# Kernel tuning notes

Hardware: AMD Instinct MI355X
Metric: run time of the kernel (lower is better)

Reference implementation:

```python
import jax, jax.numpy as jnp
import numpy as np

N_NODES = 131072
N_EDGES = 262144
N_GRAPHS = 4096
EMB = 300
N_LAYERS = 5
N_TASKS = 12
N_EXPERTS = 8
GATE_DIM = 300
NUM_ATOM_TYPE = 120
NUM_CHIRALITY = 3
NUM_BOND_TYPE = 6
NUM_BOND_DIR = 3


def setup_inputs() -> dict:
    key = jax.random.key(0)
    ks = jax.random.split(key, 24)
    x = jnp.stack([
        jax.random.randint(ks[0], (N_NODES,), 0, NUM_ATOM_TYPE),
        jax.random.randint(ks[1], (N_NODES,), 0, NUM_CHIRALITY),
    ], axis=1)
    edge_index = jax.random.randint(ks[2], (2, N_EDGES), 0, N_NODES)
    edge_attr = jnp.stack([
        jax.random.randint(ks[3], (N_EDGES,), 0, NUM_BOND_TYPE),
        jax.random.randint(ks[4], (N_EDGES,), 0, NUM_BOND_DIR),
    ], axis=1)
    batch = jnp.sort(jax.random.randint(ks[5], (N_NODES,), 0, N_GRAPHS))

    s = 0.05
    atom_emb1 = jax.random.normal(ks[6], (NUM_ATOM_TYPE, EMB)) * s
    atom_emb2 = jax.random.normal(ks[7], (NUM_CHIRALITY, EMB)) * s
    edge_emb1 = jax.random.normal(ks[8], (N_LAYERS, NUM_BOND_TYPE, EMB)) * s
    edge_emb2 = jax.random.normal(ks[9], (N_LAYERS, NUM_BOND_DIR, EMB)) * s
    mlp_w1 = jax.random.normal(ks[10], (N_LAYERS, EMB, 2 * EMB)) * s
    mlp_b1 = jnp.zeros((N_LAYERS, 2 * EMB))
    mlp_w2 = jax.random.normal(ks[11], (N_LAYERS, 2 * EMB, EMB)) * s
    mlp_b2 = jnp.zeros((N_LAYERS, EMB))
    bn_gamma = jnp.ones((N_LAYERS, EMB))
    bn_beta = jnp.zeros((N_LAYERS, EMB))
    gate_w1 = jax.random.normal(ks[12], (EMB, GATE_DIM)) * s
    gate_b1 = jnp.zeros((GATE_DIM,))
    gate_bn_g = jnp.ones((GATE_DIM,))
    gate_bn_b = jnp.zeros((GATE_DIM,))
    gate_w2 = jax.random.normal(ks[13], (GATE_DIM, GATE_DIM)) * s
    gate_b2 = jnp.zeros((GATE_DIM,))
    cluster = jax.random.normal(ks[14], (N_EXPERTS, GATE_DIM)) * s
    experts_w = jax.random.normal(ks[15], (EMB, N_TASKS * N_EXPERTS)) * s
    experts_b = jnp.zeros((N_TASKS * N_EXPERTS,))
    return dict(x=x, edge_index=edge_index, edge_attr=edge_attr, batch=batch,
                atom_emb1=atom_emb1, atom_emb2=atom_emb2,
                edge_emb1=edge_emb1, edge_emb2=edge_emb2,
                mlp_w1=mlp_w1, mlp_b1=mlp_b1, mlp_w2=mlp_w2, mlp_b2=mlp_b2,
                bn_gamma=bn_gamma, bn_beta=bn_beta,
                gate_w1=gate_w1, gate_b1=gate_b1,
                gate_bn_g=gate_bn_g, gate_bn_b=gate_bn_b,
                gate_w2=gate_w2, gate_b2=gate_b2,
                cluster=cluster, experts_w=experts_w, experts_b=experts_b)


def _batchnorm(h, g, b, eps=1e-5):
    mu = h.mean(axis=0)
    var = h.var(axis=0)
    return g * (h - mu) * jax.lax.rsqrt(var + eps) + b


def _forward(x, edge_index, edge_attr, batch,
             atom_emb1, atom_emb2, edge_emb1, edge_emb2,
             mlp_w1, mlp_b1, mlp_w2, mlp_b2, bn_gamma, bn_beta,
             gate_w1, gate_b1, gate_bn_g, gate_bn_b, gate_w2, gate_b2,
             cluster, experts_w, experts_b):
    n = x.shape[0]
    src, dst = edge_index[0], edge_index[1]
    ea0, ea1 = edge_attr[:, 0], edge_attr[:, 1]
    # node input embedding
    h = atom_emb1[x[:, 0]] + atom_emb2[x[:, 1]]  # [N, EMB]
    n_layers = mlp_w1.shape[0]
    for l in range(n_layers):
        ee = edge_emb1[l][ea0] + edge_emb2[l][ea1]  # [E, EMB]
        # self loops: attr = (bond_type=4, dir=0) for every node
        self_ee = edge_emb1[l][4] + edge_emb2[l][0]  # [EMB]
        agg = jax.ops.segment_sum(h[src] + ee, dst, num_segments=n)
        agg = agg + h + self_ee  # self-loop messages
        hid = jax.nn.relu(agg @ mlp_w1[l] + mlp_b1[l])
        h = hid @ mlp_w2[l] + mlp_b2[l]
        h = _batchnorm(h, bn_gamma[l], bn_beta[l])
        if l < n_layers - 1:
            h = jax.nn.relu(h)
    # graph pooling (JK='last')
    sums = jax.ops.segment_sum(h, batch, num_segments=N_GRAPHS)  # [B, EMB]
    counts = jax.ops.segment_sum(jnp.ones((n, 1), h.dtype), batch, num_segments=N_GRAPHS)
    gnn_out = sums / jnp.maximum(counts, 1.0)  # mean pool
    gate_input = sums  # global_add_pool
    # experts head: sum(gnn_out[:, :, None] * W, dim=1) + b == gnn_out @ W + b
    n_experts = cluster.shape[0]
    clf_logit = (gnn_out @ experts_w + experts_b).reshape(N_GRAPHS, -1, n_experts)
    # gate network
    zh = _batchnorm(gate_input @ gate_w1 + gate_b1, gate_bn_g, gate_bn_b)
    z = jax.nn.relu(zh) @ gate_w2 + gate_b2  # [B, GATE_DIM]
    # q: temperature-scaled softmax over cosine similarity to cluster centroids
    zn = z / jnp.maximum(jnp.linalg.norm(z, axis=1, keepdims=True), 1e-6)
    cn = cluster / jnp.maximum(jnp.linalg.norm(cluster, axis=1, keepdims=True), 1e-6)
    q = jax.nn.softmax(10.0 * (zn @ cn.T), axis=-1)  # T = 10
    return clf_logit, z, q


def reference(x, edge_index, edge_attr, batch,
              atom_emb1, atom_emb2, edge_emb1, edge_emb2,
              mlp_w1, mlp_b1, mlp_w2, mlp_b2, bn_gamma, bn_beta,
              gate_w1, gate_b1, gate_bn_g, gate_bn_b, gate_w2, gate_b2,
              cluster, experts_w, experts_b):
    return _forward(x, edge_index, edge_attr, batch,
                    atom_emb1, atom_emb2, edge_emb1, edge_emb2,
                    mlp_w1, mlp_b1, mlp_w2, mlp_b2, bn_gamma, bn_beta,
                    gate_w1, gate_b1, gate_bn_g, gate_bn_b, gate_w2, gate_b2,
                    cluster, experts_w, experts_b)
```

## Files before the change

kernel.cpp:

```cpp
#include <hip/hip_runtime.h>
#include <hip/hip_bf16.h>

typedef unsigned short u16;
typedef unsigned int u32;

#define NN 131072
#define NE 262144
#define NG 4096
#define EMB 300
#define HID 600
#define NL 5
#define NTNE 96
#define NEXP 8

#define W1T_ROWS 640
#define W1T_K    328
#define W2T_ROWS 384
#define W2T_K    648
#define EE_S     304

typedef __attribute__((ext_vector_type(8)))  short  s16x8;
typedef __attribute__((ext_vector_type(8)))  __bf16 b16x8;
typedef __attribute__((ext_vector_type(16))) float  f32x16;

static __device__ __forceinline__ float u2f(u16 u) {
    union { u32 i; float f; } w; w.i = ((u32)u) << 16; return w.f;
}
static __device__ __forceinline__ u16 f2u(float f) {
    union { float f; u32 i; } w; w.f = f;
    return (u16)((w.i + 0x7fffu + ((w.i >> 16) & 1u)) >> 16);
}

static __device__ __forceinline__ f32x16 mfma_3216(s16x8 a, s16x8 b, f32x16 c) {
    return __builtin_amdgcn_mfma_f32_32x32x16_bf16(
        __builtin_bit_cast(b16x8, a), __builtin_bit_cast(b16x8, b), c, 0, 0, 0);
}

__global__ void k_zero(float* __restrict__ p, int n) {
    int i = blockIdx.x * 256 + threadIdx.x;
    if (i < n) p[i] = 0.f;
}
__global__ void k_zero_int(int* __restrict__ p, int n) {
    int i = blockIdx.x * 256 + threadIdx.x;
    if (i < n) p[i] = 0;
}

__global__ void k_embed(const int* __restrict__ x, const float* __restrict__ ae1,
                        const float* __restrict__ ae2, u16* __restrict__ h) {
    int i = blockIdx.x;
    int a0 = x[2 * i], a1 = x[2 * i + 1];
    for (int f = threadIdx.x; f < EMB; f += blockDim.x)
        h[(size_t)i * EMB + f] = f2u(ae1[a0 * EMB + f] + ae2[a1 * EMB + f]);
}

__global__ void k_hist(const int* __restrict__ ei, int* __restrict__ deg) {
    int e = blockIdx.x * 256 + threadIdx.x;
    if (e < NE) atomicAdd(&deg[ei[NE + e]], 1);
}

__global__ __launch_bounds__(1024) void k_scan(const int* __restrict__ deg,
                                               int* __restrict__ rowstart) {
    __shared__ int lds[1024];
    int tid = threadIdx.x;
    int base = tid * 128;
    int s = 0;
    for (int j = 0; j < 128; ++j) s += deg[base + j];
    lds[tid] = s;
    __syncthreads();
    for (int off = 1; off < 1024; off <<= 1) {
        int v = (tid >= off) ? lds[tid - off] : 0;
        __syncthreads();
        lds[tid] += v;
        __syncthreads();
    }
    int run = (tid == 0) ? 0 : lds[tid - 1];
    for (int j = 0; j < 128; ++j) {
        rowstart[base + j] = run;
        run += deg[base + j];
    }
    if (tid == 1023) rowstart[NN] = run;
}

__global__ void k_fill(const int* __restrict__ ei, const int* __restrict__ ea,
                       int* __restrict__ deg, const int* __restrict__ rowstart,
                       u32* __restrict__ payload) {
    int e = blockIdx.x * 256 + threadIdx.x;
    if (e >= NE) return;
    int src = ei[e], dst = ei[NE + e];
    int c = ea[2 * e] * 3 + ea[2 * e + 1];
    int old = atomicSub(&deg[dst], 1);
    int pos = rowstart[dst] + old - 1;
    payload[pos] = (u32)src | ((u32)c << 17);
}

__global__ void k_prep_w1(const float* __restrict__ w1, u16* __restrict__ w1t) {
    int n = blockIdx.x;
    int l = blockIdx.y;
    size_t dst = ((size_t)l * W1T_ROWS + n) * W1T_K;
    for (int k = threadIdx.x; k < W1T_K; k += blockDim.x) {
        u16 v = 0;
        if (n < HID && k < EMB) v = f2u(w1[(size_t)l * EMB * HID + (size_t)k * HID + n]);
        w1t[dst + k] = v;
    }
}
__global__ void k_prep_w2(const float* __restrict__ w2, u16* __restrict__ w2t) {
    int n = blockIdx.x;
    int l = blockIdx.y;
    size_t dst = ((size_t)l * W2T_ROWS + n) * W2T_K;
    for (int k = threadIdx.x; k < W2T_K; k += blockDim.x) {
        u16 v = 0;
        if (n < EMB && k < HID) v = f2u(w2[(size_t)l * HID * EMB + (size_t)k * EMB + n]);
        w2t[dst + k] = v;
    }
}

__global__ void k_prep_ee(const float* __restrict__ ee1, const float* __restrict__ ee2,
                          u16* __restrict__ eeT) {
    int c = blockIdx.x;
    int l = blockIdx.y;
    size_t dst = ((size_t)l * 18 + c) * EE_S;
    const float* e1 = ee1 + (size_t)l * 6 * EMB + (c / 3) * EMB;
    const float* e2 = ee2 + (size_t)l * 3 * EMB + (c % 3) * EMB;
    for (int f = threadIdx.x; f < EE_S; f += blockDim.x)
        eeT[dst + f] = (f < EMB) ? f2u(e1[f] + e2[f]) : (u16)0;
}

__global__ void k_prep_bn(const float* __restrict__ stats, const float* __restrict__ bg,
                          const float* __restrict__ bb, float invM,
                          u16* __restrict__ scT, u16* __restrict__ shT) {
    int t = threadIdx.x;
    if (t >= EE_S) return;
    if (t < EMB) {
        float mu = stats[t] * invM;
        float var = stats[EMB + t] * invM - mu * mu;
        float sc = bg[t] * rsqrtf(var + 1e-5f);
        scT[t] = f2u(sc);
        shT[t] = f2u(bb[t] - mu * sc);
    } else {
        scT[t] = 0; shT[t] = 0;
    }
}

template <bool APPLY_BN>
__global__ __launch_bounds__(512) void k_layer1(const u16* __restrict__ h,
                                                const u32* __restrict__ payload,
                                                const int* __restrict__ rowstart,
                                                const u16* __restrict__ eeT,
                                                const u16* __restrict__ scT,
                                                const u16* __restrict__ shT,
                                                const u16* __restrict__ w1t,
                                                const float* __restrict__ b1,
                                                u16* __restrict__ hid) {
    __shared__ __align__(16) u16 A_s[64 * 328];
    int tid = threadIdx.x;
    int lane = tid & 63, wid = tid >> 6;
    int wr = wid >> 2, wc = wid & 3;
    int l31 = lane & 31, lhi = lane >> 5;
    size_t rowBase = (size_t)blockIdx.x * 64;

    for (int idx = tid; idx < 64 * 28; idx += 512)
        A_s[(idx / 28) * 328 + 300 + (idx % 28)] = 0;
    __syncthreads();

    for (int task = tid; task < 32 * 75; task += 512) {
        int pr = task / 75, fc = task - pr * 75;
        int f0 = fc * 4;
        int iA = (int)rowBase + pr;
        int iB = iA + 32;
        int begA = rowstart[iA], endA = rowstart[iA + 1];
        int begB = rowstart[iB], endB = rowstart[iB + 1];
        float sc0 = 1.f, sc1 = 1.f, sc2 = 1.f, sc3 = 1.f;
        float sh0 = 0.f, sh1 = 0.f, sh2 = 0.f, sh3 = 0.f;
        if (APPLY_BN) {
            ushort4 scv = *(const ushort4*)&scT[f0];
            ushort4 shv = *(const ushort4*)&shT[f0];
            sc0 = u2f(scv.x); sc1 = u2f(scv.y); sc2 = u2f(scv.z); sc3 = u2f(scv.w);
            sh0 = u2f(shv.x); sh1 = u2f(shv.y); sh2 = u2f(shv.z); sh3 = u2f(shv.w);
        }
        ushort4 ev = *(const ushort4*)&eeT[12 * EE_S + f0];
        float e0 = u2f(ev.x), e1v = u2f(ev.y), e2v = u2f(ev.z), e3 = u2f(ev.w);

        ushort4 hvA = *(const ushort4*)&h[(size_t)iA * EMB + f0];
        ushort4 hvB = *(const ushort4*)&h[(size_t)iB * EMB + f0];
        float vA0 = u2f(hvA.x), vA1 = u2f(hvA.y), vA2 = u2f(hvA.z), vA3 = u2f(hvA.w);
        float vB0 = u2f(hvB.x), vB1 = u2f(hvB.y), vB2 = u2f(hvB.z), vB3 = u2f(hvB.w);
        if (APPLY_BN) {
            vA0 = fmaxf(vA0 * sc0 + sh0, 0.f); vB0 = fmaxf(vB0 * sc0 + sh0, 0.f);
            vA1 = fmaxf(vA1 * sc1 + sh1, 0.f); vB1 = fmaxf(vB1 * sc1 + sh1, 0.f);
            vA2 = fmaxf(vA2 * sc2 + sh2, 0.f); vB2 = fmaxf(vB2 * sc2 + sh2, 0.f);
            vA3 = fmaxf(vA3 * sc3 + sh3, 0.f); vB3 = fmaxf(vB3 * sc3 + sh3, 0.f);
        }
        vA0 += e0; vA1 += e1v; vA2 += e2v; vA3 += e3;
        vB0 += e0; vB1 += e1v; vB2 += e2v; vB3 += e3;

        int eA = begA, eB = begB;
        while (eA < endA && eB < endB) {
            u32 pA = payload[eA], pB = payload[eB];
            int sA = pA & 0x1FFFF, sB = pB & 0x1FFFF;
            ushort4 svA = *(const ushort4*)&h[(size_t)sA * EMB + f0];
            ushort4 svB = *(const ushort4*)&h[(size_t)sB * EMB + f0];
            ushort4 ecA = *(const ushort4*)&eeT[(size_t)(pA >> 17) * EE_S + f0];
            ushort4 ecB = *(const ushort4*)&eeT[(size_t)(pB >> 17) * EE_S + f0];
            float gA0 = u2f(svA.x), gA1 = u2f(svA.y), gA2 = u2f(svA.z), gA3 = u2f(svA.w);
            float gB0 = u2f(svB.x), gB1 = u2f(svB.y), gB2 = u2f(svB.z), gB3 = u2f(svB.w);
            if (APPLY_BN) {
                gA0 = fmaxf(gA0 * sc0 + sh0, 0.f); gB0 = fmaxf(gB0 * sc0 + sh0, 0.f);
                gA1 = fmaxf(gA1 * sc1 + sh1, 0.f); gB1 = fmaxf(gB1 * sc1 + sh1, 0.f);
                gA2 = fmaxf(gA2 * sc2 + sh2, 0.f); gB2 = fmaxf(gB2 * sc2 + sh2, 0.f);
                gA3 = fmaxf(gA3 * sc3 + sh3, 0.f); gB3 = fmaxf(gB3 * sc3 + sh3, 0.f);
            }
            vA0 += gA0 + u2f(ecA.x); vB0 += gB0 + u2f(ecB.x);
            vA1 += gA1 + u2f(ecA.y); vB1 += gB1 + u2f(ecB.y);
            vA2 += gA2 + u2f(ecA.z); vB2 += gB2 + u2f(ecB.z);
            vA3 += gA3 + u2f(ecA.w); vB3 += gB3 + u2f(ecB.w);
            ++eA; ++eB;
        }
        for (; eA < endA; ++eA) {
            u32 p = payload[eA];
            int src = p & 0x1FFFF;
            ushort4 sv = *(const ushort4*)&h[(size_t)src * EMB + f0];
            ushort4 ec = *(const ushort4*)&eeT[(size_t)(p >> 17) * EE_S + f0];
            float g0 = u2f(sv.x), g1 = u2f(sv.y), g2 = u2f(sv.z), g3 = u2f(sv.w);
            if (APPLY_BN) {
                g0 = fmaxf(g0 * sc0 + sh0, 0.f);
                g1 = fmaxf(g1 * sc1 + sh1, 0.f);
                g2 = fmaxf(g2 * sc2 + sh2, 0.f);
                g3 = fmaxf(g3 * sc3 + sh3, 0.f);
            }
            vA0 += g0 + u2f(ec.x);
            vA1 += g1 + u2f(ec.y);
            vA2 += g2 + u2f(ec.z);
            vA3 += g3 + u2f(ec.w);
        }
        for (; eB < endB; ++eB) {
            u32 p = payload[eB];
            int src = p & 0x1FFFF;
            ushort4 sv = *(const ushort4*)&h[(size_t)src * EMB + f0];
            ushort4 ec = *(const ushort4*)&eeT[(size_t)(p >> 17) * EE_S + f0];
            float g0 = u2f(sv.x), g1 = u2f(sv.y), g2 = u2f(sv.z), g3 = u2f(sv.w);
            if (APPLY_BN) {
                g0 = fmaxf(g0 * sc0 + sh0, 0.f);
                g1 = fmaxf(g1 * sc1 + sh1, 0.f);
                g2 = fmaxf(g2 * sc2 + sh2, 0.f);
                g3 = fmaxf(g3 * sc3 + sh3, 0.f);
            }
            vB0 += g0 + u2f(ec.x);
            vB1 += g1 + u2f(ec.y);
            vB2 += g2 + u2f(ec.z);
            vB3 += g3 + u2f(ec.w);
        }
        short4 oA, oB;
        oA.x = (short)f2u(vA0); oA.y = (short)f2u(vA1);
        oA.z = (short)f2u(vA2); oA.w = (short)f2u(vA3);
        oB.x = (short)f2u(vB0); oB.y = (short)f2u(vB1);
        oB.z = (short)f2u(vB2); oB.w = (short)f2u(vB3);
        *(short4*)&A_s[pr * 328 + f0] = oA;
        *(short4*)&A_s[(pr + 32) * 328 + f0] = oB;
    }
    __syncthreads();

    s16x8 afr[20];
    int abase = (wr * 32 + l31) * 328 + lhi * 8;
#pragma unroll
    for (int s = 0; s < 20; ++s) afr[s] = *(const s16x8*)&A_s[abase + s * 16];

    for (int c5 = 0; c5 < 5; ++c5) {
        int col = c5 * 128 + wc * 32 + l31;
        const u16* bp = w1t + (size_t)col * W1T_K + lhi * 8;
        f32x16 acc = {};
#pragma unroll
        for (int s = 0; s < 20; ++s)
            acc = mfma_3216(afr[s], *(const s16x8*)&bp[s * 16], acc);
        if (col < HID) {
            float bias = b1[col];
#pragma unroll
            for (int r = 0; r < 16; ++r) {
                int row = (r & 3) + 8 * (r >> 2) + 4 * lhi;
                hid[(rowBase + wr * 32 + row) * HID + col] =
                    f2u(fmaxf(acc[r] + bias, 0.f));
            }
        }
    }
}

__global__ __launch_bounds__(256) void k_gemm2(const u16* __restrict__ hid,
                                               const u16* __restrict__ w2t,
                                               const float* __restrict__ b2,
                                               u16* __restrict__ hout) {
    __shared__ __align__(16) u16 A_s[64 * 72];
    __shared__ __align__(16) u16 B_s[128 * 72];
    int tid = threadIdx.x;
    int lane = tid & 63, wid = tid >> 6;
    int wr = wid >> 1, wc = wid & 1;
    int l31 = lane & 31, lhi = lane >> 5;
    size_t rowBase = (size_t)blockIdx.x * 64;
    int cc = blockIdx.y * 128;

    f32x16 acc0 = {}, acc1 = {};
    int aoff = (wr * 32 + l31) * 72 + lhi * 8;
    int boff0 = (wc * 64 + l31) * 72 + lhi * 8;
    int boff1 = boff0 + 32 * 72;

    for (int sl = 0; sl < 10; ++sl) {
        int k0 = sl * 64;
        for (int idx = tid; idx < 512; idx += 256) {
            int m = idx >> 3, kv = idx & 7;
            int k = k0 + kv * 8;
            s16x8 v = {};
            if (k < HID) v = *(const s16x8*)&hid[(rowBase + m) * HID + k];
            *(s16x8*)&A_s[m * 72 + kv * 8] = v;
        }
        for (int idx = tid; idx < 1024; idx += 256) {
            int n = idx >> 3, kv = idx & 7;
            *(s16x8*)&B_s[n * 72 + kv * 8] =
                *(const s16x8*)&w2t[(size_t)(cc + n) * W2T_K + k0 + kv * 8];
        }
        __syncthreads();

        int smax = (sl < 9) ? 4 : 2;
        for (int s = 0; s < smax; ++s) {
            s16x8 a  = *(const s16x8*)&A_s[aoff + s * 16];
            s16x8 ba = *(const s16x8*)&B_s[boff0 + s * 16];
            s16x8 bb = *(const s16x8*)&B_s[boff1 + s * 16];
            acc0 = mfma_3216(a, ba, acc0);
            acc1 = mfma_3216(a, bb, acc1);
        }
        __syncthreads();
    }

    int colA = cc + wc * 64 + l31;
    int colB = colA + 32;
    if (colA < EMB) {
        float bias = b2[colA];
#pragma unroll
        for (int r = 0; r < 16; ++r) {
            int row = (r & 3) + 8 * (r >> 2) + 4 * lhi;
            hout[(rowBase + wr * 32 + row) * EMB + colA] = f2u(acc0[r] + bias);
        }
    }
    if (colB < EMB) {
        float bias = b2[colB];
#pragma unroll
        for (int r = 0; r < 16; ++r) {
            int row = (r & 3) + 8 * (r >> 2) + 4 * lhi;
            hout[(rowBase + wr * 32 + row) * EMB + colB] = f2u(acc1[r] + bias);
        }
    }
}

__global__ void k_bn_stats_h(const u16* __restrict__ X, float* __restrict__ stats) {
    int t = threadIdx.x;
    int half = t / 160;
    int pr = t - half * 160;
    if (pr >= 150) return;
    float s0 = 0.f, s1 = 0.f, q0 = 0.f, q1 = 0.f;
    for (int r = blockIdx.x * 2 + half; r < NN; r += 512) {
        u32 v = *(const u32*)&X[(size_t)r * EMB + pr * 2];
        float a = u2f((u16)(v & 0xffff));
        float b = u2f((u16)(v >> 16));
        s0 += a; s1 += b; q0 += a * a; q1 += b * b;
    }
    atomicAdd(&stats[2 * pr], s0);
    atomicAdd(&stats[2 * pr + 1], s1);
    atomicAdd(&stats[EMB + 2 * pr], q0);
    atomicAdd(&stats[EMB + 2 * pr + 1], q1);
}

template <bool RELU>
__global__ void k_bn_apply_h(u16* __restrict__ X, const float* __restrict__ stats,
                             const float* __restrict__ g, const float* __restrict__ b, float invM) {
    int r = blockIdx.x;
    for (int f = threadIdx.x; f < EMB; f += blockDim.x) {
        float mu = stats[f] * invM;
        float var = stats[EMB + f] * invM - mu * mu;
        float v = (u2f(X[(size_t)r * EMB + f]) - mu) * rsqrtf(var + 1e-5f) * g[f] + b[f];
        if (RELU) v = fmaxf(v, 0.f);
        X[(size_t)r * EMB + f] = f2u(v);
    }
}

__global__ void k_bn_stats_f(const float* __restrict__ X, int M, float* __restrict__ stats) {
    int f = threadIdx.x;
    if (f >= EMB) return;
    float s = 0.f, s2 = 0.f;
    for (int r = blockIdx.x; r < M; r += gridDim.x) {
        float v = X[(size_t)r * EMB + f];
        s += v;
        s2 += v * v;
    }
    atomicAdd(&stats[f], s);
    atomicAdd(&stats[EMB + f], s2);
}

template <bool RELU>
__global__ void k_bn_apply_f(float* __restrict__ X, const float* __restrict__ stats,
                             const float* __restrict__ g, const float* __restrict__ b, float invM) {
    int r = blockIdx.x;
    for (int f = threadIdx.x; f < EMB; f += blockDim.x) {
        float mu = stats[f] * invM;
        float var = stats[EMB + f] * invM - mu * mu;
        float v = (X[(size_t)r * EMB + f] - mu) * rsqrtf(var + 1e-5f) * g[f] + b[f];
        if (RELU) v = fmaxf(v, 0.f);
        X[(size_t)r * EMB + f] = v;
    }
}

template <bool RELU>
__global__ __launch_bounds__(256) void k_gemm(const float* __restrict__ A,
                                              const float* __restrict__ B,
                                              const float* __restrict__ bias,
                                              float* __restrict__ C, int M, int N, int K) {
    __shared__ __align__(16) float As[16][68];
    __shared__ __align__(16) float Bs[16][68];
    int tid = threadIdx.x;
    int tx = tid & 15, ty = tid >> 4;
    int rowBase = blockIdx.y * 64;
    int colBase = blockIdx.x * 64;
    float acc[4][4] = {};
    for (int k0 = 0; k0 < K; k0 += 16) {
        for (int idx = tid; idx < 1024; idx += 256) {
            int m = idx >> 4, k = idx & 15;
            int gk = k0 + k;
            As[k][m] = (gk < K) ? A[(size_t)(rowBase + m) * K + gk] : 0.f;
        }
        for (int idx = tid; idx < 1024; idx += 256) {
            int kk = idx >> 6, n = idx & 63;
            int gk = k0 + kk, gn = colBase + n;
            Bs[kk][n] = (gk < K && gn < N) ? B[(size_t)gk * N + gn] : 0.f;
        }
        __syncthreads();
#pragma unroll
        for (int k = 0; k < 16; ++k) {
            const float* ar = &As[k][ty * 4];
            const float* br = &Bs[k][tx * 4];
            float a[4], b[4];
#pragma unroll
            for (int i = 0; i < 4; ++i) a[i] = ar[i];
#pragma unroll
            for (int j = 0; j < 4; ++j) b[j] = br[j];
#pragma unroll
            for (int i = 0; i < 4; ++i)
#pragma unroll
                for (int j = 0; j < 4; ++j) acc[i][j] += a[i] * b[j];
        }
        __syncthreads();
    }
#pragma unroll
    for (int i = 0; i < 4; ++i) {
        int r = rowBase + ty * 4 + i;
#pragma unroll
        for (int j = 0; j < 4; ++j) {
            int c = colBase + tx * 4 + j;
            if (c < N && r < M) {
                float v = acc[i][j] + bias[c];
                if (RELU) v = fmaxf(v, 0.f);
                C[(size_t)r * N + c] = v;
            }
        }
    }
}

__global__ void k_pool(const u16* __restrict__ h, const int* __restrict__ batch,
                       float* __restrict__ sums, float* __restrict__ counts) {
    __shared__ int range[2];
    int g = blockIdx.x;
    int t = threadIdx.x;
    if (t < 2) {
        int target = g + t;
        int lo = 0, hi = NN;
        while (lo < hi) {
            int mid = (lo + hi) >> 1;
            if (batch[mid] < target) lo = mid + 1; else hi = mid;
        }
        range[t] = lo;
    }
    __syncthreads();
    int beg = range[0], end = range[1];
    if (t < EMB) {
        float s = 0.f;
        for (int r = beg; r < end; ++r) s += u2f(h[(size_t)r * EMB + t]);
        sums[(size_t)g * EMB + t] = s;
    }
    if (t == 0) counts[g] = (float)(end - beg);
}

__global__ void k_clf(const float* __restrict__ sums, const float* __restrict__ counts,
                      const float* __restrict__ ew, const float* __restrict__ eb,
                      float* __restrict__ out) {
    int gi = blockIdx.x;
    int t = threadIdx.x;
    if (t >= NTNE) return;
    float cnt = fmaxf(counts[gi], 1.f);
    float acc = 0.f;
    for (int k = 0; k < EMB; ++k) acc += sums[(size_t)gi * EMB + k] * ew[k * NTNE + t];
    out[(size_t)gi * NTNE + t] = acc / cnt + eb[t];
}

__global__ void k_cnorm(const float* __restrict__ cluster, float* __restrict__ cnorm) {
    int l = threadIdx.x;
    for (int e = 0; e < NEXP; ++e) {
        float s = 0.f;
        for (int f = l; f < EMB; f += 64) {
            float v = cluster[e * EMB + f];
            s += v * v;
        }
        for (int o = 32; o; o >>= 1) s += __shfl_xor(s, o);
        if (l == 0) cnorm[e] = sqrtf(s);
    }
}

__global__ void k_zout(const float* __restrict__ z, float* __restrict__ out) {
    int gi = blockIdx.x;
    for (int f = threadIdx.x; f < EMB; f += blockDim.x)
        out[(size_t)gi * EMB + f] = z[(size_t)gi * EMB + f];
}

__global__ void k_q(const float* __restrict__ z, const float* __restrict__ cluster,
                    const float* __restrict__ cnorm, float* __restrict__ qout) {
    int gi = blockIdx.x;
    int l = threadIdx.x;
    float s = 0.f;
    for (int f = l; f < EMB; f += 64) {
        float v = z[(size_t)gi * EMB + f];
        s += v * v;
    }
    for (int o = 32; o; o >>= 1) s += __shfl_xor(s, o);
    float zn = fmaxf(sqrtf(s), 1e-6f);
    float sc[NEXP];
#pragma unroll
    for (int e = 0; e < NEXP; ++e) {
        float d = 0.f;
        for (int f = l; f < EMB; f += 64) d += z[(size_t)gi * EMB + f] * cluster[e * EMB + f];
        for (int o = 32; o; o >>= 1) d += __shfl_xor(d, o);
        sc[e] = 10.f * d / (zn * fmaxf(cnorm[e], 1e-6f));
    }
    float mx = sc[0];
#pragma unroll
    for (int e = 1; e < NEXP; ++e) mx = fmaxf(mx, sc[e]);
    float se = 0.f;
#pragma unroll
    for (int e = 0; e < NEXP; ++e) {
        sc[e] = expf(sc[e] - mx);
        se += sc[e];
    }
    if (l < NEXP) qout[(size_t)gi * NEXP + l] = sc[l] / se;
}

extern "C" void kernel_launch(void* const* d_in, const int* in_sizes, int n_in,
                              void* d_out, int out_size, void* d_ws, size_t ws_size,
                              hipStream_t stream) {
    const int* x       = (const int*)d_in[0];
    const int* ei      = (const int*)d_in[1];
    const int* ea      = (const int*)d_in[2];
    const int* batch   = (const int*)d_in[3];
    const float* ae1   = (const float*)d_in[4];
    const float* ae2   = (const float*)d_in[5];
    const float* ee1   = (const float*)d_in[6];
    const float* ee2   = (const float*)d_in[7];
    const float* w1    = (const float*)d_in[8];
    const float* b1    = (const float*)d_in[9];
    const float* w2    = (const float*)d_in[10];
    const float* b2    = (const float*)d_in[11];
    const float* bng   = (const float*)d_in[12];
    const float* bnb   = (const float*)d_in[13];
    const float* gw1   = (const float*)d_in[14];
    const float* gb1   = (const float*)d_in[15];
    const float* gbng  = (const float*)d_in[16];
    const float* gbnb  = (const float*)d_in[17];
    const float* gw2   = (const float*)d_in[18];
    const float* gb2   = (const float*)d_in[19];
    const float* clus  = (const float*)d_in[20];
    const float* ew    = (const float*)d_in[21];
    const float* eb    = (const float*)d_in[22];

    char* wp = (char*)d_ws;
    u16* hbuf = (u16*)wp;                 wp += (size_t)NN * EMB * sizeof(u16);
    u16* hid = (u16*)wp;                  wp += (size_t)NN * HID * sizeof(u16);
    float* stats = (float*)wp;            wp += 2 * EMB * sizeof(float);
    u16* w1t = (u16*)wp;                  wp += (size_t)NL * W1T_ROWS * W1T_K * sizeof(u16);
    u16* w2t = (u16*)wp;                  wp += (size_t)NL * W2T_ROWS * W2T_K * sizeof(u16);
    u16* eeT = (u16*)wp;                  wp += (size_t)NL * 18 * EE_S * sizeof(u16);
    u16* scT = (u16*)wp;                  wp += EE_S * sizeof(u16);
    u16* shT = (u16*)wp;                  wp += EE_S * sizeof(u16);
    int* deg = (int*)wp;                  wp += (size_t)NN * sizeof(int);
    int* rowstart = (int*)wp;             wp += (size_t)(NN + 4) * sizeof(int);
    u32* payload = (u32*)wp;              wp += (size_t)NE * sizeof(u32);

    float* sums   = (float*)hid;
    float* counts = sums + (size_t)NG * EMB;
    float* zh     = counts + NG;
    float* zb     = zh + (size_t)NG * EMB;
    float* cnorm  = zb + (size_t)NG * EMB;

    float* out     = (float*)d_out;
    float* out_clf = out;
    float* out_z   = out + (size_t)NG * NTNE;
    float* out_q   = out_z + (size_t)NG * EMB;

    k_zero_int<<<NN / 256, 256, 0, stream>>>(deg, NN);
    k_hist<<<NE / 256, 256, 0, stream>>>(ei, deg);
    k_scan<<<1, 1024, 0, stream>>>(deg, rowstart);
    k_fill<<<NE / 256, 256, 0, stream>>>(ei, ea, deg, rowstart, payload);

    k_prep_w1<<<dim3(W1T_ROWS, NL), 64, 0, stream>>>(w1, w1t);
    k_prep_w2<<<dim3(W2T_ROWS, NL), 64, 0, stream>>>(w2, w2t);
    k_prep_ee<<<dim3(18, NL), 128, 0, stream>>>(ee1, ee2, eeT);
    k_embed<<<NN, 320, 0, stream>>>(x, ae1, ae2, hbuf);

    for (int l = 0; l < NL; ++l) {
        const u16* eeL = eeT + (size_t)l * 18 * EE_S;
        if (l == 0)
            k_layer1<false><<<NN / 64, 512, 0, stream>>>(
                hbuf, payload, rowstart, eeL, nullptr, nullptr,
                w1t + (size_t)l * W1T_ROWS * W1T_K, b1 + (size_t)l * HID, hid);
        else
            k_layer1<true><<<NN / 64, 512, 0, stream>>>(
                hbuf, payload, rowstart, eeL, scT, shT,
                w1t + (size_t)l * W1T_ROWS * W1T_K, b1 + (size_t)l * HID, hid);
        k_gemm2<<<dim3(NN / 64, 3), 256, 0, stream>>>(hid, w2t + (size_t)l * W2T_ROWS * W2T_K,
                                                      b2 + (size_t)l * EMB, hbuf);
        k_zero<<<3, 256, 0, stream>>>(stats, 2 * EMB);
        k_bn_stats_h<<<256, 320, 0, stream>>>(hbuf, stats);
        if (l < NL - 1)
            k_prep_bn<<<1, 320, 0, stream>>>(stats, bng + (size_t)l * EMB,
                                             bnb + (size_t)l * EMB, 1.f / NN, scT, shT);
    }

    k_bn_apply_h<false><<<NN, 320, 0, stream>>>(hbuf, stats, bng + (size_t)(NL - 1) * EMB,
                                                bnb + (size_t)(NL - 1) * EMB, 1.f / NN);

    k_pool<<<NG, 320, 0, stream>>>(hbuf, batch, sums, counts);
    k_clf<<<NG, 128, 0, stream>>>(sums, counts, ew, eb, out_clf);

    k_gemm<false><<<dim3(5, NG / 64), 256, 0, stream>>>(sums, gw1, gb1, zh, NG, EMB, EMB);
    k_zero<<<3, 256, 0, stream>>>(stats, 2 * EMB);
    k_bn_stats_f<<<256, 320, 0, stream>>>(zh, NG, stats);
    k_bn_apply_f<true><<<NG, 320, 0, stream>>>(zh, stats, gbng, gbnb, 1.f / NG);
    k_gemm<false><<<dim3(5, NG / 64), 256, 0, stream>>>(zh, gw2, gb2, zb, NG, EMB, EMB);

    k_cnorm<<<1, 64, 0, stream>>>(clus, cnorm);
    k_zout<<<NG, 320, 0, stream>>>(zb, out_z);
    k_q<<<NG, 64, 0, stream>>>(zb, clus, cnorm, out_q);
}
```

Before: 3.006 ms.

## Compute all output columns per gemm2 block and use nontemporal hid traffic

The second MLP GEMM now has each 64-row block compute all 384 padded output columns, with six accumulators per wave, instead of splitting columns across three blocks. Each hidden-activation tile is therefore read once rather than three times, at the cost of a 3x larger weight tile in LDS (about 64KB total), more registers, and a third as many blocks. The hidden-activation stores in gemm1 and loads in gemm2 also use nontemporal hints to reduce cache pollution.

```diff
diff --git a/kernel.cpp b/kernel.cpp
--- a/kernel.cpp
+++ b/kernel.cpp
@@ -276,8 +276,9 @@
 #pragma unroll
             for (int r = 0; r < 16; ++r) {
                 int row = (r & 3) + 8 * (r >> 2) + 4 * lhi;
-                hid[(rowBase + wr * 32 + row) * HID + col] =
-                    f2u(fmaxf(acc[r] + bias, 0.f));
+                u16 val = f2u(fmaxf(acc[r] + bias, 0.f));
+                __builtin_nontemporal_store(val,
+                    &hid[(rowBase + wr * 32 + row) * HID + col]);
             }
         }
     }
@@ -288,18 +289,16 @@
                                                const float* __restrict__ b2,
                                                u16* __restrict__ hout) {
     __shared__ __align__(16) u16 A_s[64 * 72];
-    __shared__ __align__(16) u16 B_s[128 * 72];
+    __shared__ __align__(16) u16 B_s[384 * 72];
     int tid = threadIdx.x;
     int lane = tid & 63, wid = tid >> 6;
-    int wr = wid >> 1, wc = wid & 1;
+    int wr = wid >> 1, wcg = wid & 1;
     int l31 = lane & 31, lhi = lane >> 5;
     size_t rowBase = (size_t)blockIdx.x * 64;
-    int cc = blockIdx.y * 128;
-
-    f32x16 acc0 = {}, acc1 = {};
+
+    f32x16 acc0 = {}, acc1 = {}, acc2 = {}, acc3 = {}, acc4 = {}, acc5 = {};
     int aoff = (wr * 32 + l31) * 72 + lhi * 8;
-    int boff0 = (wc * 64 + l31) * 72 + lhi * 8;
-    int boff1 = boff0 + 32 * 72;
+    int bbase = (wcg * 192 + l31) * 72 + lhi * 8;
 
     for (int sl = 0; sl < 10; ++sl) {
         int k0 = sl * 64;
@@ -307,45 +306,46 @@
             int m = idx >> 3, kv = idx & 7;
             int k = k0 + kv * 8;
             s16x8 v = {};
-            if (k < HID) v = *(const s16x8*)&hid[(rowBase + m) * HID + k];
+            if (k < HID)
+                v = __builtin_nontemporal_load(
+                        (const s16x8*)&hid[(rowBase + m) * HID + k]);
             *(s16x8*)&A_s[m * 72 + kv * 8] = v;
         }
-        for (int idx = tid; idx < 1024; idx += 256) {
+        for (int idx = tid; idx < 3072; idx += 256) {
             int n = idx >> 3, kv = idx & 7;
             *(s16x8*)&B_s[n * 72 + kv * 8] =
-                *(const s16x8*)&w2t[(size_t)(cc + n) * W2T_K + k0 + kv * 8];
+                *(const s16x8*)&w2t[(size_t)n * W2T_K + k0 + kv * 8];
         }
         __syncthreads();
 
         int smax = (sl < 9) ? 4 : 2;
         for (int s = 0; s < smax; ++s) {
-            s16x8 a  = *(const s16x8*)&A_s[aoff + s * 16];
-            s16x8 ba = *(const s16x8*)&B_s[boff0 + s * 16];
-            s16x8 bb = *(const s16x8*)&B_s[boff1 + s * 16];
-            acc0 = mfma_3216(a, ba, acc0);
-            acc1 = mfma_3216(a, bb, acc1);
+            s16x8 a = *(const s16x8*)&A_s[aoff + s * 16];
+            acc0 = mfma_3216(a, *(const s16x8*)&B_s[bbase + 0 * 32 * 72 + s * 16], acc0);
+            acc1 = mfma_3216(a, *(const s16x8*)&B_s[bbase + 1 * 32 * 72 + s * 16], acc1);
+            acc2 = mfma_3216(a, *(const s16x8*)&B_s[bbase + 2 * 32 * 72 + s * 16], acc2);
+            acc3 = mfma_3216(a, *(const s16x8*)&B_s[bbase + 3 * 32 * 72 + s * 16], acc3);
+            acc4 = mfma_3216(a, *(const s16x8*)&B_s[bbase + 4 * 32 * 72 + s * 16], acc4);
+            acc5 = mfma_3216(a, *(const s16x8*)&B_s[bbase + 5 * 32 * 72 + s * 16], acc5);
         }
         __syncthreads();
     }
 
-    int colA = cc + wc * 64 + l31;
-    int colB = colA + 32;
-    if (colA < EMB) {
-        float bias = b2[colA];
-#pragma unroll
-        for (int r = 0; r < 16; ++r) {
-            int row = (r & 3) + 8 * (r >> 2) + 4 * lhi;
-            hout[(rowBase + wr * 32 + row) * EMB + colA] = f2u(acc0[r] + bias);
-        }
-    }
-    if (colB < EMB) {
-        float bias = b2[colB];
-#pragma unroll
-        for (int r = 0; r < 16; ++r) {
-            int row = (r & 3) + 8 * (r >> 2) + 4 * lhi;
-            hout[(rowBase + wr * 32 + row) * EMB + colB] = f2u(acc1[r] + bias);
-        }
-    }
+#define WRITE_SUB(ACC, SUB)                                                     \
+    {                                                                           \
+        int col = wcg * 192 + (SUB) * 32 + l31;                                 \
+        if (col < EMB) {                                                        \
+            float bias = b2[col];                                               \
+            _Pragma("unroll")                                                   \
+            for (int r = 0; r < 16; ++r) {                                      \
+                int row = (r & 3) + 8 * (r >> 2) + 4 * lhi;                     \
+                hout[(rowBase + wr * 32 + row) * EMB + col] = f2u(ACC[r] + bias); \
+            }                                                                   \
+        }                                                                       \
+    }
+    WRITE_SUB(acc0, 0) WRITE_SUB(acc1, 1) WRITE_SUB(acc2, 2)
+    WRITE_SUB(acc3, 3) WRITE_SUB(acc4, 4) WRITE_SUB(acc5, 5)
+#undef WRITE_SUB
 }
 
 __global__ void k_bn_stats_h(const u16* __restrict__ X, float* __restrict__ stats) {
@@ -617,8 +617,8 @@
             k_layer1<true><<<NN / 64, 512, 0, stream>>>(
                 hbuf, payload, rowstart, eeL, scT, shT,
                 w1t + (size_t)l * W1T_ROWS * W1T_K, b1 + (size_t)l * HID, hid);
-        k_gemm2<<<dim3(NN / 64, 3), 256, 0, stream>>>(hid, w2t + (size_t)l * W2T_ROWS * W2T_K,
-                                                      b2 + (size_t)l * EMB, hbuf);
+        k_gemm2<<<NN / 64, 256, 0, stream>>>(hid, w2t + (size_t)l * W2T_ROWS * W2T_K,
+                                             b2 + (size_t)l * EMB, hbuf);
         k_zero<<<3, 256, 0, stream>>>(stats, 2 * EMB);
         k_bn_stats_h<<<256, 320, 0, stream>>>(hbuf, stats);
         if (l < NL - 1)
```

After: 3.162 ms. 1.05x slower.
